# Kernel tuning notes

Hardware: AMD Instinct MI355X
Metric: run time of the kernel (lower is better)

## Reference

```python
import jax, jax.numpy as jnp
import numpy as np


def setup_inputs() -> dict:
    key = jax.random.key(0)
    ks = jax.random.split(key, 4)
    B, T, D, H, E = 4, 2048, 1024, 4096, 8
    s = 0.02
    x = jax.random.normal(ks[0], (B, T, D), dtype=jnp.float32)
    Wr = jax.random.normal(ks[1], (D, E), dtype=jnp.float32) * s
    br = jnp.zeros((E,), dtype=jnp.float32)
    W1 = jax.random.normal(ks[2], (E, D, H), dtype=jnp.float32) * s
    b1 = jnp.zeros((E, H), dtype=jnp.float32)
    W2 = jax.random.normal(ks[3], (E, H, D), dtype=jnp.float32) * s
    b2 = jnp.zeros((E, D), dtype=jnp.float32)
    return {"x": x, "Wr": Wr, "br": br, "W1": W1, "b1": b1, "W2": W2, "b2": b2}


def reference(x, Wr, br, W1, b1, W2, b2):
    # Router: top-1 selection
    logits = jnp.einsum('btd,de->bte', x, Wr) + br            # [B,T,E]
    probs = jax.nn.softmax(logits, axis=-1)                   # [B,T,E]
    expert_idx = jnp.argmax(probs, axis=-1)                   # [B,T] int
    E = W1.shape[0]
    onehot = jax.nn.one_hot(expert_idx, E, dtype=x.dtype)     # [B,T,E]
    # Dense grouped-MLP over all experts, then combine with one-hot routing.
    # h: [B,E,T,H]
    h = jax.nn.relu(jnp.einsum('btd,edh->beth', x, W1) + b1[None, :, None, :])
    y = jnp.einsum('beth,ehd->betd', h, W2) + b2[None, :, None, :]  # [B,E,T,D]
    out = jnp.einsum('bte,betd->btd', onehot, y)              # [B,T,D]
    return out, probs, expert_idx
```

## Files before the change

### kernel.cpp

```cpp
#include <hip/hip_runtime.h>

#define NTOK 8192
#define DD 1024
#define HH 4096
#define EE 8
#define MAXBLK 72

typedef __attribute__((ext_vector_type(8))) short bf16x8;
typedef __attribute__((ext_vector_type(4))) float f32x4;

__device__ __forceinline__ unsigned short f2bf(float f) {
  unsigned u = __builtin_bit_cast(unsigned, f);
  u += 0x7fffu + ((u >> 16) & 1u);
  return (unsigned short)(u >> 16);
}

union Pack8 {
  unsigned short u[8];
  uint4 v;
};

__device__ __forceinline__ void gload_lds16(const void* g, void* l) {
  __builtin_amdgcn_global_load_lds(
      (const __attribute__((address_space(1))) unsigned int*)g,
      (__attribute__((address_space(3))) unsigned int*)l, 16, 0, 0);
}

__global__ __launch_bounds__(256) void k_router(
    const float* __restrict__ x, const float* __restrict__ Wr,
    const float* __restrict__ br, float* __restrict__ probs,
    float* __restrict__ idxf, int* __restrict__ idxi,
    unsigned short* __restrict__ xb) {
  const int lane = threadIdx.x & 63;
  const int token = blockIdx.x * 4 + (threadIdx.x >> 6);
  const float* xr = x + (size_t)token * DD;

  float acc[EE];
#pragma unroll
  for (int e = 0; e < EE; ++e) acc[e] = 0.f;

#pragma unroll
  for (int i = 0; i < 4; ++i) {
    const int d0 = i * 256 + lane * 4;
    const float4 xv = *reinterpret_cast<const float4*>(xr + d0);
    union { unsigned short u[4]; uint2 v; } pk;
    pk.u[0] = f2bf(xv.x); pk.u[1] = f2bf(xv.y);
    pk.u[2] = f2bf(xv.z); pk.u[3] = f2bf(xv.w);
    *reinterpret_cast<uint2*>(xb + (size_t)token * DD + d0) = pk.v;
    const float xs[4] = {xv.x, xv.y, xv.z, xv.w};
#pragma unroll
    for (int j = 0; j < 4; ++j) {
      const float xd = xs[j];
      const float4 w0 = *reinterpret_cast<const float4*>(Wr + (size_t)(d0 + j) * EE);
      const float4 w1 = *reinterpret_cast<const float4*>(Wr + (size_t)(d0 + j) * EE + 4);
      acc[0] += xd * w0.x; acc[1] += xd * w0.y; acc[2] += xd * w0.z; acc[3] += xd * w0.w;
      acc[4] += xd * w1.x; acc[5] += xd * w1.y; acc[6] += xd * w1.z; acc[7] += xd * w1.w;
    }
  }
#pragma unroll
  for (int s = 32; s > 0; s >>= 1) {
#pragma unroll
    for (int e = 0; e < EE; ++e) acc[e] += __shfl_xor(acc[e], s, 64);
  }

  float lg[EE];
#pragma unroll
  for (int e = 0; e < EE; ++e) lg[e] = acc[e] + br[e];

  int best = 0;
  float bv = lg[0];
#pragma unroll
  for (int e = 1; e < EE; ++e) {
    if (lg[e] > bv) { bv = lg[e]; best = e; }
  }
  float p[EE], s = 0.f;
#pragma unroll
  for (int e = 0; e < EE; ++e) { p[e] = expf(lg[e] - bv); s += p[e]; }
  const float inv = 1.f / s;

  if (lane == 0) {
#pragma unroll
    for (int e = 0; e < EE; ++e) probs[(size_t)token * EE + e] = p[e] * inv;
    idxf[token] = (float)best;
    idxi[token] = best;
  }
}

__global__ __launch_bounds__(512) void k_compact(const int* __restrict__ idxi,
                                                 int* __restrict__ cnt,
                                                 int* __restrict__ off,
                                                 int* __restrict__ sorted,
                                                 int* __restrict__ meta) {
  __shared__ int sidx[NTOK];
  __shared__ int scnt[EE], soff[EE];
  const int tid = threadIdx.x;
  for (int i = tid; i < NTOK; i += 512) sidx[i] = idxi[i];
  __syncthreads();
  const int w = tid >> 6, lane = tid & 63;
  if (w < EE) {
    int c = 0;
    for (int i = 0; i < NTOK / 64; ++i) {
      unsigned long long m = __ballot(sidx[i * 64 + lane] == w);
      c += __popcll(m);
    }
    if (lane == 0) scnt[w] = c;
  }
  __syncthreads();
  if (tid == 0) {
    int s = 0;
    for (int e = 0; e < EE; ++e) { soff[e] = s; s += scnt[e]; }
    int nb = 0;
    for (int e = 0; e < EE; ++e) {
      const int nmb = (scnt[e] + 127) >> 7;
      for (int m = 0; m < nmb; ++m) {
        meta[16 + nb] = e;
        meta[96 + nb] = m << 7;
        ++nb;
      }
    }
    meta[0] = nb;
  }
  __syncthreads();
  if (w < EE) {
    int base = soff[w];
    const unsigned long long ltmask = (1ull << lane) - 1ull;
    for (int i = 0; i < NTOK / 64; ++i) {
      const int tok = i * 64 + lane;
      const bool f = (sidx[tok] == w);
      unsigned long long m = __ballot(f);
      if (f) {
        int r = __popcll(m & ltmask);
        sorted[base + r] = tok;
      }
      base += __popcll(m);
    }
    if (lane == 0) { cnt[w] = scnt[w]; off[w] = soff[w]; }
  }
}

__global__ __launch_bounds__(256) void k_trcvt64(const float* __restrict__ in,
                                                 unsigned short* __restrict__ outp,
                                                 int R, int C) {
  const int e = blockIdx.z;
  const int r0 = blockIdx.y * 64, c0 = blockIdx.x * 64;
  const float* src = in + (size_t)e * R * C + (size_t)r0 * C + c0;
  unsigned short* dst = outp + (size_t)e * R * C + (size_t)c0 * R + r0;
  __shared__ unsigned short t[64 * 66];
  const int tid = threadIdx.x;
#pragma unroll
  for (int it = 0; it < 4; ++it) {
    const int r = it * 16 + (tid >> 4), c4 = (tid & 15) * 4;
    const float4 v = *reinterpret_cast<const float4*>(src + (size_t)r * C + c4);
    t[r * 66 + c4 + 0] = f2bf(v.x);
    t[r * 66 + c4 + 1] = f2bf(v.y);
    t[r * 66 + c4 + 2] = f2bf(v.z);
    t[r * 66 + c4 + 3] = f2bf(v.w);
  }
  __syncthreads();
#pragma unroll
  for (int it = 0; it < 2; ++it) {
    const int cc = it * 32 + (tid >> 3), r8 = (tid & 7) * 8;
    Pack8 p;
#pragma unroll
    for (int j = 0; j < 8; ++j) p.u[j] = t[(r8 + j) * 66 + cc];
    *reinterpret_cast<uint4*>(dst + (size_t)cc * R + r8) = p.v;
  }
}

__global__ __launch_bounds__(256) void k_gemm1n(
    const unsigned short* __restrict__ xb, const unsigned short* __restrict__ W1t,
    const float* __restrict__ b1, const int* __restrict__ meta,
    const int* __restrict__ cnt, const int* __restrict__ off,
    const int* __restrict__ sorted, unsigned short* __restrict__ h) {
  const int bid = blockIdx.x;
  if (bid >= meta[0]) return;
  const int e = meta[16 + bid];
  const int m0 = meta[96 + bid];
  const int c = cnt[e], base = off[e];
  const int n0 = blockIdx.y * 128;

  __shared__ __align__(16) unsigned short Al[128 * 64];
  __shared__ __align__(16) unsigned short Bl[128 * 64];

  const int tid = threadIdx.x, l = tid & 63, w = tid >> 6;

  const unsigned short* aptr[4];
  const unsigned short* bptr[4];
  int soff4[4];
#pragma unroll
  for (int i = 0; i < 4; ++i) {
    const int r = i * 32 + w * 8 + (l >> 3);
    const int swz = ((l & 7) ^ (r & 7)) * 8;
    int ar = m0 + r; if (ar >= c) ar = c - 1;
    const int tok = sorted[base + ar];
    aptr[i] = xb + (size_t)tok * DD + swz;
    bptr[i] = W1t + ((size_t)e * HH + n0 + r) * DD + swz;
    soff4[i] = r * 64 + (l & 7) * 8;
  }

  const int lr = l & 15, lg = l >> 4;
  const int wr = w >> 1, wc = w & 1;
  int aoff[4], boff[4], asw[4], bsw[4];
#pragma unroll
  for (int m = 0; m < 4; ++m) {
    int row = wr * 64 + m * 16 + lr;
    aoff[m] = row * 64; asw[m] = row & 7;
    row = wc * 64 + m * 16 + lr;
    boff[m] = row * 64; bsw[m] = row & 7;
  }

  f32x4 acc[4][4];
#pragma unroll
  for (int m = 0; m < 4; ++m)
#pragma unroll
    for (int n = 0; n < 4; ++n) acc[m][n] = {0.f, 0.f, 0.f, 0.f};

  for (int k0 = 0; k0 < DD; k0 += 64) {
    __syncthreads();
#pragma unroll
    for (int i = 0; i < 4; ++i) gload_lds16(aptr[i] + k0, &Al[soff4[i]]);
#pragma unroll
    for (int i = 0; i < 4; ++i) gload_lds16(bptr[i] + k0, &Bl[soff4[i]]);
    __syncthreads();
#pragma unroll
    for (int ks = 0; ks < 2; ++ks) {
      bf16x8 af[4], bv[4];
#pragma unroll
      for (int m = 0; m < 4; ++m)
        af[m] = *reinterpret_cast<const bf16x8*>(&Al[aoff[m] + (((ks * 4 + lg) ^ asw[m]) * 8)]);
#pragma unroll
      for (int n = 0; n < 4; ++n)
        bv[n] = *reinterpret_cast<const bf16x8*>(&Bl[boff[n] + (((ks * 4 + lg) ^ bsw[n]) * 8)]);
#pragma unroll
      for (int m = 0; m < 4; ++m)
#pragma unroll
        for (int n = 0; n < 4; ++n)
          acc[m][n] = __builtin_amdgcn_mfma_f32_16x16x32_bf16(af[m], bv[n], acc[m][n], 0, 0, 0);
    }
  }

  const int valid = c - m0;
#pragma unroll
  for (int m = 0; m < 4; ++m) {
#pragma unroll
    for (int rr = 0; rr < 4; ++rr) {
      const int tr = wr * 64 + m * 16 + lg * 4 + rr;
      if (tr < valid) {
        const size_t row = (size_t)(base + m0 + tr);
#pragma unroll
        for (int n = 0; n < 4; ++n) {
          const int col = n0 + wc * 64 + n * 16 + lr;
          const float v = acc[m][n][rr] + b1[e * HH + col];
          h[row * HH + col] = f2bf(fmaxf(v, 0.f));
        }
      }
    }
  }
}

__global__ __launch_bounds__(512) void k_gemm2s(
    const unsigned short* __restrict__ h, const unsigned short* __restrict__ W2t,
    const float* __restrict__ b2, const int* __restrict__ meta,
    const int* __restrict__ cnt, const int* __restrict__ off,
    const int* __restrict__ sorted, float* __restrict__ out) {
  const int bid = blockIdx.x;
  if (bid >= meta[0]) return;
  const int e = meta[16 + bid];
  const int m0 = meta[96 + bid];
  const int c = cnt[e], base = off[e];
  const int n0 = blockIdx.y * 128;

  __shared__ __align__(16) unsigned short LDSU[4][128 * 64];

  const int tid = threadIdx.x, l = tid & 63;
  const int w = tid >> 6;
  const int g = w >> 2;
  const int wg = w & 3;

  const unsigned short* aptr[4];
  const unsigned short* bptr[4];
  int soff4[4];
#pragma unroll
  for (int i = 0; i < 4; ++i) {
    const int r = i * 32 + wg * 8 + (l >> 3);
    const int swz = ((l & 7) ^ (r & 7)) * 8;
    int ar = m0 + r; if (ar >= c) ar = c - 1;
    aptr[i] = h + (size_t)(base + ar) * HH + g * 2048 + swz;
    bptr[i] = W2t + ((size_t)e * DD + n0 + r) * HH + g * 2048 + swz;
    soff4[i] = r * 64 + (l & 7) * 8;
  }

  const int lr = l & 15, lg = l >> 4;
  const int wr = wg >> 1, wc = wg & 1;
  int aoff[4], boff[4], asw[4], bsw[4];
#pragma unroll
  for (int m = 0; m < 4; ++m) {
    int row = wr * 64 + m * 16 + lr;
    aoff[m] = row * 64; asw[m] = row & 7;
    row = wc * 64 + m * 16 + lr;
    boff[m] = row * 64; bsw[m] = row & 7;
  }

  f32x4 acc[4][4];
#pragma unroll
  for (int m = 0; m < 4; ++m)
#pragma unroll
    for (int n = 0; n < 4; ++n) acc[m][n] = {0.f, 0.f, 0.f, 0.f};

  for (int t = 0; t < 32; ++t) {
    const int k0 = t * 64;
    __syncthreads();
#pragma unroll
    for (int i = 0; i < 4; ++i) gload_lds16(aptr[i] + k0, &LDSU[g][soff4[i]]);
#pragma unroll
    for (int i = 0; i < 4; ++i) gload_lds16(bptr[i] + k0, &LDSU[2 + g][soff4[i]]);
    __syncthreads();
#pragma unroll
    for (int ks = 0; ks < 2; ++ks) {
      bf16x8 af[4], bv[4];
#pragma unroll
      for (int m = 0; m < 4; ++m)
        af[m] = *reinterpret_cast<const bf16x8*>(&LDSU[g][aoff[m] + (((ks * 4 + lg) ^ asw[m]) * 8)]);
#pragma unroll
      for (int n = 0; n < 4; ++n)
        bv[n] = *reinterpret_cast<const bf16x8*>(&LDSU[2 + g][boff[n] + (((ks * 4 + lg) ^ bsw[n]) * 8)]);
#pragma unroll
      for (int m = 0; m < 4; ++m)
#pragma unroll
        for (int n = 0; n < 4; ++n)
          acc[m][n] = __builtin_amdgcn_mfma_f32_16x16x32_bf16(af[m], bv[n], acc[m][n], 0, 0, 0);
    }
  }

  __syncthreads();
  float* red = (float*)LDSU;
  if (g == 1) {
#pragma unroll
    for (int m = 0; m < 4; ++m)
#pragma unroll
      for (int rr = 0; rr < 4; ++rr) {
        const int row = wr * 64 + m * 16 + lg * 4 + rr;
#pragma unroll
        for (int n = 0; n < 4; ++n) {
          const int col = wc * 64 + n * 16 + lr;
          red[row * 128 + col] = acc[m][n][rr];
        }
      }
  }
  __syncthreads();
  if (g == 0) {
    const int valid = c - m0;
#pragma unroll
    for (int m = 0; m < 4; ++m) {
#pragma unroll
      for (int rr = 0; rr < 4; ++rr) {
        const int tr = wr * 64 + m * 16 + lg * 4 + rr;
        if (tr < valid) {
          const int token = sorted[base + m0 + tr];
#pragma unroll
          for (int n = 0; n < 4; ++n) {
            const int col = wc * 64 + n * 16 + lr;
            out[(size_t)token * DD + n0 + col] =
                acc[m][n][rr] + red[tr * 128 + col] + b2[e * DD + n0 + col];
          }
        }
      }
    }
  }
}

extern "C" void kernel_launch(void* const* d_in, const int* in_sizes, int n_in,
                              void* d_out, int out_size, void* d_ws, size_t ws_size,
                              hipStream_t stream) {
  const float* x  = (const float*)d_in[0];
  const float* Wr = (const float*)d_in[1];
  const float* br = (const float*)d_in[2];
  const float* W1 = (const float*)d_in[3];
  const float* b1 = (const float*)d_in[4];
  const float* W2 = (const float*)d_in[5];
  const float* b2 = (const float*)d_in[6];

  float* out   = (float*)d_out;
  float* probs = out + (size_t)NTOK * DD;
  float* idxf  = probs + (size_t)NTOK * EE;

  char* ws = (char*)d_ws;
  int* cnt    = (int*)(ws + 0);
  int* off    = (int*)(ws + 64);
  int* meta   = (int*)(ws + 128);
  int* idxi   = (int*)(ws + 1024);
  int* sorted = (int*)(ws + 33792);

  const size_t OFF_XB  = 66560;
  const size_t OFF_W1T = OFF_XB + (size_t)NTOK * DD * 2;
  const size_t OFF_H   = OFF_W1T + (size_t)EE * DD * HH * 2;
  const size_t OFF_W2T = OFF_XB;

  unsigned short* xb  = (unsigned short*)(ws + OFF_XB);
  unsigned short* W1t = (unsigned short*)(ws + OFF_W1T);
  unsigned short* W2t = (unsigned short*)(ws + OFF_W2T);
  unsigned short* h   = (unsigned short*)(ws + OFF_H);

  k_router<<<NTOK / 4, 256, 0, stream>>>(x, Wr, br, probs, idxf, idxi, xb);
  k_compact<<<1, 512, 0, stream>>>(idxi, cnt, off, sorted, meta);
  k_trcvt64<<<dim3(HH / 64, DD / 64, EE), 256, 0, stream>>>(W1, W1t, DD, HH);
  k_gemm1n<<<dim3(MAXBLK, HH / 128), 256, 0, stream>>>(xb, W1t, b1, meta, cnt, off, sorted, h);
  k_trcvt64<<<dim3(DD / 64, HH / 64, EE), 256, 0, stream>>>(W2, W2t, HH, DD);
  k_gemm2s<<<dim3(MAXBLK, DD / 128), 512, 0, stream>>>(h, W2t, b2, meta, cnt, off, sorted, out);
}
```

Baseline: 400.3 us.

## Swap grid axes for row-tile reuse and replace split-K GEMM2 with narrow tiles

Both grouped GEMMs now put the N-tile index on blockIdx.x, so consecutive blocks share the same token row tile of A, which should improve L2 reuse of xb/h. GEMM2 drops the 512-thread split-K scheme and its LDS reduction. Instead it uses 256-thread blocks computing 128x64 tiles over the full K, which doubles the N-tile count to restore parallelism. The cost is a longer K loop per block and halved B reuse per A tile loaded.

Result: faster. 375.0 us (-6.3%).

```diff
diff --git a/kernel.cpp b/kernel.cpp
--- a/kernel.cpp
+++ b/kernel.cpp
@@ -172,12 +172,12 @@
     const float* __restrict__ b1, const int* __restrict__ meta,
     const int* __restrict__ cnt, const int* __restrict__ off,
     const int* __restrict__ sorted, unsigned short* __restrict__ h) {
-  const int bid = blockIdx.x;
+  const int bid = blockIdx.y;
   if (bid >= meta[0]) return;
   const int e = meta[16 + bid];
   const int m0 = meta[96 + bid];
   const int c = cnt[e], base = off[e];
-  const int n0 = blockIdx.y * 128;
+  const int n0 = blockIdx.x * 128;
 
   __shared__ __align__(16) unsigned short Al[128 * 64];
   __shared__ __align__(16) unsigned short Bl[128 * 64];
@@ -258,111 +258,98 @@
   }
 }
 
-__global__ __launch_bounds__(512) void k_gemm2s(
+__global__ __launch_bounds__(256) void k_gemm2w(
     const unsigned short* __restrict__ h, const unsigned short* __restrict__ W2t,
     const float* __restrict__ b2, const int* __restrict__ meta,
     const int* __restrict__ cnt, const int* __restrict__ off,
     const int* __restrict__ sorted, float* __restrict__ out) {
-  const int bid = blockIdx.x;
+  const int bid = blockIdx.y;
   if (bid >= meta[0]) return;
   const int e = meta[16 + bid];
   const int m0 = meta[96 + bid];
   const int c = cnt[e], base = off[e];
-  const int n0 = blockIdx.y * 128;
-
-  __shared__ __align__(16) unsigned short LDSU[4][128 * 64];
-
-  const int tid = threadIdx.x, l = tid & 63;
-  const int w = tid >> 6;
-  const int g = w >> 2;
-  const int wg = w & 3;
+  const int n0 = blockIdx.x * 64;
+
+  __shared__ __align__(16) unsigned short Al[128 * 64];
+  __shared__ __align__(16) unsigned short Bl[64 * 64];
+
+  const int tid = threadIdx.x, l = tid & 63, w = tid >> 6;
 
   const unsigned short* aptr[4];
-  const unsigned short* bptr[4];
-  int soff4[4];
+  const unsigned short* bptr[2];
+  int asoff[4], bsoff[2];
 #pragma unroll
   for (int i = 0; i < 4; ++i) {
-    const int r = i * 32 + wg * 8 + (l >> 3);
+    const int r = i * 32 + w * 8 + (l >> 3);
     const int swz = ((l & 7) ^ (r & 7)) * 8;
     int ar = m0 + r; if (ar >= c) ar = c - 1;
-    aptr[i] = h + (size_t)(base + ar) * HH + g * 2048 + swz;
-    bptr[i] = W2t + ((size_t)e * DD + n0 + r) * HH + g * 2048 + swz;
-    soff4[i] = r * 64 + (l & 7) * 8;
+    aptr[i] = h + (size_t)(base + ar) * HH + swz;
+    asoff[i] = r * 64 + (l & 7) * 8;
+  }
+#pragma unroll
+  for (int i = 0; i < 2; ++i) {
+    const int r = i * 32 + w * 8 + (l >> 3);
+    const int swz = ((l & 7) ^ (r & 7)) * 8;
+    bptr[i] = W2t + ((size_t)e * DD + n0 + r) * HH + swz;
+    bsoff[i] = r * 64 + (l & 7) * 8;
   }
 
   const int lr = l & 15, lg = l >> 4;
-  const int wr = wg >> 1, wc = wg & 1;
-  int aoff[4], boff[4], asw[4], bsw[4];
+  const int wr = w >> 1, wc = w & 1;
+  int aoff[4], boff[2], asw[4], bsw[2];
 #pragma unroll
   for (int m = 0; m < 4; ++m) {
-    int row = wr * 64 + m * 16 + lr;
+    const int row = wr * 64 + m * 16 + lr;
     aoff[m] = row * 64; asw[m] = row & 7;
-    row = wc * 64 + m * 16 + lr;
-    boff[m] = row * 64; bsw[m] = row & 7;
-  }
-
-  f32x4 acc[4][4];
+  }
+#pragma unroll
+  for (int n = 0; n < 2; ++n) {
+    const int row = wc * 32 + n * 16 + lr;
+    boff[n] = row * 64; bsw[n] = row & 7;
+  }
+
+  f32x4 acc[4][2];
 #pragma unroll
   for (int m = 0; m < 4; ++m)
 #pragma unroll
-    for (int n = 0; n < 4; ++n) acc[m][n] = {0.f, 0.f, 0.f, 0.f};
-
-  for (int t = 0; t < 32; ++t) {
-    const int k0 = t * 64;
+    for (int n = 0; n < 2; ++n) acc[m][n] = {0.f, 0.f, 0.f, 0.f};
+
+  for (int k0 = 0; k0 < HH; k0 += 64) {
     __syncthreads();
 #pragma unroll
-    for (int i = 0; i < 4; ++i) gload_lds16(aptr[i] + k0, &LDSU[g][soff4[i]]);
-#pragma unroll
-    for (int i = 0; i < 4; ++i) gload_lds16(bptr[i] + k0, &LDSU[2 + g][soff4[i]]);
+    for (int i = 0; i < 4; ++i) gload_lds16(aptr[i] + k0, &Al[asoff[i]]);
+#pragma unroll
+    for (int i = 0; i < 2; ++i) gload_lds16(bptr[i] + k0, &Bl[bsoff[i]]);
     __syncthreads();
 #pragma unroll
     for (int ks = 0; ks < 2; ++ks) {
-      bf16x8 af[4], bv[4];
+      bf16x8 af[4], bv[2];
 #pragma unroll
       for (int m = 0; m < 4; ++m)
-        af[m] = *reinterpret_cast<const bf16x8*>(&LDSU[g][aoff[m] + (((ks * 4 + lg) ^ asw[m]) * 8)]);
-#pragma unroll
-      for (int n = 0; n < 4; ++n)
-        bv[n] = *reinterpret_cast<const bf16x8*>(&LDSU[2 + g][boff[n] + (((ks * 4 + lg) ^ bsw[n]) * 8)]);
+        af[m] = *reinterpret_cast<const bf16x8*>(&Al[aoff[m] + (((ks * 4 + lg) ^ asw[m]) * 8)]);
+#pragma unroll
+      for (int n = 0; n < 2; ++n)
+        bv[n] = *reinterpret_cast<const bf16x8*>(&Bl[boff[n] + (((ks * 4 + lg) ^ bsw[n]) * 8)]);
 #pragma unroll
       for (int m = 0; m < 4; ++m)
 #pragma unroll
-        for (int n = 0; n < 4; ++n)
+        for (int n = 0; n < 2; ++n)
           acc[m][n] = __builtin_amdgcn_mfma_f32_16x16x32_bf16(af[m], bv[n], acc[m][n], 0, 0, 0);
     }
   }
 
-  __syncthreads();
-  float* red = (float*)LDSU;
-  if (g == 1) {
-#pragma unroll
-    for (int m = 0; m < 4; ++m)
-#pragma unroll
-      for (int rr = 0; rr < 4; ++rr) {
-        const int row = wr * 64 + m * 16 + lg * 4 + rr;
-#pragma unroll
-        for (int n = 0; n < 4; ++n) {
-          const int col = wc * 64 + n * 16 + lr;
-          red[row * 128 + col] = acc[m][n][rr];
-        }
-      }
-  }
-  __syncthreads();
-  if (g == 0) {
-    const int valid = c - m0;
-#pragma unroll
-    for (int m = 0; m < 4; ++m) {
-#pragma unroll
-      for (int rr = 0; rr < 4; ++rr) {
-        const int tr = wr * 64 + m * 16 + lg * 4 + rr;
-        if (tr < valid) {
-          const int token = sorted[base + m0 + tr];
-#pragma unroll
-          for (int n = 0; n < 4; ++n) {
-            const int col = wc * 64 + n * 16 + lr;
-            out[(size_t)token * DD + n0 + col] =
-                acc[m][n][rr] + red[tr * 128 + col] + b2[e * DD + n0 + col];
-          }
+  const int valid = c - m0;
+#pragma unroll
+  for (int m = 0; m < 4; ++m) {
+#pragma unroll
+    for (int rr = 0; rr < 4; ++rr) {
+      const int tr = wr * 64 + m * 16 + lg * 4 + rr;
+      if (tr < valid) {
+        const int token = sorted[base + m0 + tr];
+#pragma unroll
+        for (int n = 0; n < 2; ++n) {
+          const int col = n0 + wc * 32 + n * 16 + lr;
+          out[(size_t)token * DD + col] = acc[m][n][rr] + b2[e * DD + col];
         }
       }
     }
@@ -404,7 +391,7 @@
   k_router<<<NTOK / 4, 256, 0, stream>>>(x, Wr, br, probs, idxf, idxi, xb);
   k_compact<<<1, 512, 0, stream>>>(idxi, cnt, off, sorted, meta);
   k_trcvt64<<<dim3(HH / 64, DD / 64, EE), 256, 0, stream>>>(W1, W1t, DD, HH);
-  k_gemm1n<<<dim3(MAXBLK, HH / 128), 256, 0, stream>>>(xb, W1t, b1, meta, cnt, off, sorted, h);
+  k_gemm1n<<<dim3(HH / 128, MAXBLK), 256, 0, stream>>>(xb, W1t, b1, meta, cnt, off, sorted, h);
   k_trcvt64<<<dim3(DD / 64, HH / 64, EE), 256, 0, stream>>>(W2, W2t, HH, DD);
-  k_gemm2s<<<dim3(MAXBLK, DD / 128), 512, 0, stream>>>(h, W2t, b2, meta, cnt, off, sorted, out);
-}
+  k_gemm2w<<<dim3(DD / 64, MAXBLK), 256, 0, stream>>>(h, W2t, b2, meta, cnt, off, sorted, out);
+}
```
